# Performance work log

Hardware: AMD Instinct MI355X
Metric: run time of the kernel (lower is better)

The kernel has to match this reference:

```python
import jax, jax.numpy as jnp
import numpy as np

N, E, D, G, L = 100000, 1600000, 32, 64, 3
BN_EPS = 1e-5


def setup_inputs() -> dict:
    key = jax.random.key(0)
    ks = jax.random.split(key, 8)
    x = jax.random.normal(ks[0], (N, D), dtype=jnp.float32)
    edge_index = jax.random.randint(ks[1], (2, E), 0, N, dtype=jnp.int64)
    batch = jnp.sort(jax.random.randint(ks[2], (N,), 0, G, dtype=jnp.int64))
    layer_weights = jnp.ones((L,), dtype=jnp.float32)
    # linears[i]: Linear(D->D) + BN(D) (inference-mode stats) ; L of them
    lin_W = jax.random.normal(ks[3], (L, D, D), dtype=jnp.float32) * (1.0 / np.sqrt(D))
    lin_b = jnp.zeros((L, D), dtype=jnp.float32)
    lin_gamma = jnp.ones((L, D), dtype=jnp.float32)
    lin_beta = jnp.zeros((L, D), dtype=jnp.float32)
    lin_mean = jnp.zeros((L, D), dtype=jnp.float32)
    lin_var = jnp.ones((L, D), dtype=jnp.float32)
    # GINConv MLPs: Linear(D->D) + BN(D) + ELU ; L-1 of them
    conv_W = jax.random.normal(ks[4], (L - 1, D, D), dtype=jnp.float32) * (1.0 / np.sqrt(D))
    conv_b = jnp.zeros((L - 1, D), dtype=jnp.float32)
    conv_gamma = jnp.ones((L - 1, D), dtype=jnp.float32)
    conv_beta = jnp.zeros((L - 1, D), dtype=jnp.float32)
    conv_mean = jnp.zeros((L - 1, D), dtype=jnp.float32)
    conv_var = jnp.ones((L - 1, D), dtype=jnp.float32)
    return {"x": x, "edge_index": edge_index, "batch": batch,
            "layer_weights": layer_weights,
            "lin_W": lin_W, "lin_b": lin_b, "lin_gamma": lin_gamma,
            "lin_beta": lin_beta, "lin_mean": lin_mean, "lin_var": lin_var,
            "conv_W": conv_W, "conv_b": conv_b, "conv_gamma": conv_gamma,
            "conv_beta": conv_beta, "conv_mean": conv_mean, "conv_var": conv_var}


def _mlp(h, W, b, gamma, beta, mean, var):
    # Linear -> BatchNorm1d (inference stats) -> ELU
    h = h @ W + b
    h = (h - mean) * (gamma * jax.lax.rsqrt(var + BN_EPS)) + beta
    return jax.nn.elu(h)


def reference(x, edge_index, batch, layer_weights,
              lin_W, lin_b, lin_gamma, lin_beta, lin_mean, lin_var,
              conv_W, conv_b, conv_gamma, conv_beta, conv_mean, conv_var):
    src, dst = edge_index[0], edge_index[1]
    z = _mlp(x, lin_W[0], lin_b[0], lin_gamma[0], lin_beta[0], lin_mean[0], lin_var[0])
    Z = layer_weights[0] * z
    out = jax.ops.segment_max(z, batch, num_segments=G)  # global_max_pool
    for l in range(1, L):
        # GINConv (eps=0): x' = MLP(x + sum_{j->i} x_j)
        agg = jax.ops.segment_sum(x[src], dst, num_segments=N)
        x = _mlp(x + agg, conv_W[l - 1], conv_b[l - 1], conv_gamma[l - 1],
                 conv_beta[l - 1], conv_mean[l - 1], conv_var[l - 1])
        z = layer_weights[l] * _mlp(x, lin_W[l], lin_b[l], lin_gamma[l],
                                    lin_beta[l], lin_mean[l], lin_var[l])
        Z = Z + z
        out = out + jax.ops.segment_max(z, batch, num_segments=G)
    # dropout p=0.0 is identity
    return (out, Z, x)
```

## Files before the change

### kernel.cpp

```cpp
#include <hip/hip_runtime.h>
#include <math.h>

#define N_NODES 100000
#define N_EDGES 1600000
#define DIM 32
#define N_GROUPS 64
#define BN_EPS 1e-5f

#define BIN_NODES 128
#define NBINS ((N_NODES + BIN_NODES - 1) / BIN_NODES)
#define EPB_HIST 2048
#define HIST_BLOCKS ((N_EDGES + EPB_HIST - 1) / EPB_HIST)
#define EPB_SCAT 8192
#define SCAT_SUB (EPB_SCAT / EPB_HIST)
#define SCAT_BLOCKS ((N_EDGES + EPB_SCAT - 1) / EPB_SCAT)
#define GF2_BLOCKS ((N_NODES + 127) / 128)
#define CNT_PAD 16

#define HLS 40

typedef __attribute__((ext_vector_type(8))) short short8;
typedef __attribute__((ext_vector_type(4))) float f32x4;
typedef __attribute__((ext_vector_type(4))) unsigned u32x4;

__device__ __forceinline__ unsigned enc_f32(float f) {
    unsigned u = __float_as_uint(f);
    return (u & 0x80000000u) ? ~u : (u | 0x80000000u);
}
__device__ __forceinline__ float dec_f32(unsigned u) {
    return (u & 0x80000000u) ? __uint_as_float(u & 0x7FFFFFFFu) : __uint_as_float(~u);
}
__device__ __forceinline__ unsigned short f2bf(float f) {
    unsigned u = __float_as_uint(f);
    u += 0x7FFFu + ((u >> 16) & 1u);
    return (unsigned short)(u >> 16);
}

__global__ __launch_bounds__(256) void foldhist_kernel(
        const float* __restrict__ lin_W, const float* __restrict__ lin_b,
        const float* __restrict__ lin_gamma, const float* __restrict__ lin_beta,
        const float* __restrict__ lin_mean, const float* __restrict__ lin_var,
        const float* __restrict__ conv_W, const float* __restrict__ conv_b,
        const float* __restrict__ conv_gamma, const float* __restrict__ conv_beta,
        const float* __restrict__ conv_mean, const float* __restrict__ conv_var,
        float* __restrict__ shf, unsigned short* __restrict__ Wfb,
        unsigned short* __restrict__ x0b, unsigned short* __restrict__ xbufb,
        const int* __restrict__ dst, int* __restrict__ bincnt,
        int* __restrict__ blockcnt)
{
    __shared__ int cnt[NBINS];
    int bid = blockIdx.x;
    int t = threadIdx.x;
    if (bid >= 6) {
        int hb = bid - 6;
        for (int b = t; b < NBINS; b += 256) cnt[b] = 0;
        __syncthreads();
        int base = hb * EPB_HIST;
        for (int i = 0; i < EPB_HIST / 256; ++i) {
            int e = base + i * 256 + t;
            if (e < N_EDGES) atomicAdd(&cnt[dst[e] >> 7], 1);
        }
        __syncthreads();
        for (int b = t; b < NBINS; b += 256) {
            int c = cnt[b];
            blockcnt[(size_t)hb * NBINS + b] = c;
            if (c > 0) atomicAdd(&bincnt[b * CNT_PAD], c);
        }
        return;
    }
    if (bid == 5) {
        if (t < DIM) {
            x0b[(size_t)N_NODES * DIM + t] = 0;
            xbufb[(size_t)N_NODES * DIM + t] = 0;
        }
        return;
    }
    const float *W, *b, *gm, *bt, *mn, *vr;
    if (bid < 3) {
        W = lin_W + bid * DIM * DIM; b = lin_b + bid * DIM; gm = lin_gamma + bid * DIM;
        bt = lin_beta + bid * DIM;   mn = lin_mean + bid * DIM; vr = lin_var + bid * DIM;
    } else {
        int c = bid - 3;
        W = conv_W + c * DIM * DIM; b = conv_b + c * DIM; gm = conv_gamma + c * DIM;
        bt = conv_beta + c * DIM;   mn = conv_mean + c * DIM; vr = conv_var + c * DIM;
    }
    for (int idx = t; idx < DIM * DIM; idx += 256) {
        int j = idx & (DIM - 1);
        float scale = gm[j] / sqrtf(vr[j] + BN_EPS);
        Wfb[bid * DIM * DIM + idx] = f2bf(W[idx] * scale);
    }
    if (t < DIM) {
        float scale = gm[t] / sqrtf(vr[t] + BN_EPS);
        shf[bid * DIM + t] = (b[t] - mn[t]) * scale + bt[t];
    }
}

__global__ __launch_bounds__(1024) void binscan_kernel(const int* __restrict__ bincnt,
                                                       int* __restrict__ binoff,
                                                       int* __restrict__ bincur) {
    __shared__ int s[1024];
    int t = threadIdx.x;
    int c = (t < NBINS) ? bincnt[t * CNT_PAD] : 0;
    s[t] = c;
    __syncthreads();
    for (int off = 1; off < 1024; off <<= 1) {
        int u = (t >= off) ? s[t - off] : 0;
        __syncthreads();
        s[t] += u;
        __syncthreads();
    }
    if (t < NBINS) { binoff[t] = s[t] - c; bincur[t * CNT_PAD] = s[t] - c; }
    if (t == 0) binoff[NBINS] = N_EDGES;
}

__global__ __launch_bounds__(512) void scatter_linz_kernel(
        const int* __restrict__ src, const int* __restrict__ dst,
        int* __restrict__ bincur, unsigned* __restrict__ binbuf,
        const int* __restrict__ blockcnt,
        const float* __restrict__ x0, unsigned short* __restrict__ x0b,
        const unsigned short* __restrict__ Wb, const float* __restrict__ shfv,
        const int* __restrict__ batch, const float* __restrict__ lw_ptr,
        float* __restrict__ Z, unsigned* __restrict__ segmax)
{
    __shared__ int smem[NBINS];
    int t = threadIdx.x;

    if (blockIdx.x < SCAT_BLOCKS) {
        int* pos = smem;
        for (int b = t; b < NBINS; b += 512) {
            int c = 0;
#pragma unroll
            for (int k = 0; k < SCAT_SUB; ++k) {
                int r = blockIdx.x * SCAT_SUB + k;
                if (r < HIST_BLOCKS)
                    c += blockcnt[(size_t)r * NBINS + b];
            }
            pos[b] = (c > 0) ? atomicAdd(&bincur[b * CNT_PAD], c) : 0;
        }
        __syncthreads();
        int base = blockIdx.x * EPB_SCAT;
        for (int i = 0; i < EPB_SCAT / 512; ++i) {
            int e = base + i * 512 + t;
            if (e < N_EDGES) {
                int d = dst[e];
                int bin = d >> 7;
                int p = atomicAdd(&pos[bin], 1);
                binbuf[p] = ((unsigned)(d & 127) << 17) | (unsigned)src[e];
            }
        }
        return;
    }

    unsigned* segloc = (unsigned*)smem;
    if (t < 8 * DIM) segloc[t] = 0;

    int wv = t >> 6, lane = t & 63;
    int m = lane & 15, kg = lane >> 4;

    short8 b0, b1;
#pragma unroll
    for (int j = 0; j < 8; ++j) {
        int k = kg * 8 + j;
        b0[j] = (short)Wb[k * DIM + m];
        b1[j] = (short)Wb[k * DIM + 16 + m];
    }
    float sh0 = shfv[m], sh1 = shfv[m + 16];
    float lw = lw_ptr[0];
    int blk0 = (blockIdx.x - SCAT_BLOCKS) * 128;
    int gfirst = batch[blk0];
    int row0 = blk0 + wv * 16;
    __syncthreads();

    if (row0 < N_NODES) {
        const float* rp = x0 + (size_t)(row0 + m) * DIM + kg * 8;
        f32x4 v0 = *(const f32x4*)rp;
        f32x4 v1 = *(const f32x4*)(rp + 4);
        short8 a;
        a[0] = (short)f2bf(v0[0]); a[1] = (short)f2bf(v0[1]);
        a[2] = (short)f2bf(v0[2]); a[3] = (short)f2bf(v0[3]);
        a[4] = (short)f2bf(v1[0]); a[5] = (short)f2bf(v1[1]);
        a[6] = (short)f2bf(v1[2]); a[7] = (short)f2bf(v1[3]);
        *(short8*)(x0b + (size_t)(row0 + m) * DIM + kg * 8) = a;

        f32x4 d0 = {0.f, 0.f, 0.f, 0.f}, d1 = {0.f, 0.f, 0.f, 0.f};
        d0 = __builtin_amdgcn_mfma_f32_16x16x32_bf16(a, b0, d0, 0, 0, 0);
        d1 = __builtin_amdgcn_mfma_f32_16x16x32_bf16(a, b1, d1, 0, 0, 0);
#pragma unroll
        for (int r = 0; r < 4; ++r) {
            int row = row0 + kg * 4 + r;
            float a0 = d0[r] + sh0;
            float a1 = d1[r] + sh1;
            float z0 = a0 > 0.f ? a0 : expm1f(a0);
            float z1 = a1 > 0.f ? a1 : expm1f(a1);
            size_t zi = (size_t)row * DIM;
            Z[zi + m] = lw * z0;
            Z[zi + 16 + m] = lw * z1;
            int g = batch[row];
            int go = g - gfirst;
            if (go < 8) {
                atomicMax(&segloc[go * DIM + m], enc_f32(z0));
                atomicMax(&segloc[go * DIM + 16 + m], enc_f32(z1));
            } else {
                atomicMax(&segmax[g * DIM + m], enc_f32(z0));
                atomicMax(&segmax[g * DIM + 16 + m], enc_f32(z1));
            }
        }
    }
    __syncthreads();
    if (t < 8 * DIM) {
        unsigned v = segloc[t];
        if (v) atomicMax(&segmax[(gfirst + (t >> 5)) * DIM + (t & 31)], v);
    }
}

__global__ __launch_bounds__(256) void binsort_kernel(const unsigned* __restrict__ binbuf,
                                                      const int* __restrict__ binoff,
                                                      int* __restrict__ esrc,
                                                      int* __restrict__ nodeptr) {
    __shared__ int cnt[BIN_NODES];
    __shared__ int sc[BIN_NODES];
    int t = threadIdx.x;
    int bin = blockIdx.x;
    int beg = binoff[bin], end = binoff[bin + 1];
    if (t < BIN_NODES) cnt[t] = 0;
    __syncthreads();
    for (int e = beg + t; e < end; e += 256)
        atomicAdd(&cnt[binbuf[e] >> 17], 1);
    __syncthreads();
    int v = (t < BIN_NODES) ? cnt[t] : 0;
    if (t < BIN_NODES) sc[t] = v;
    __syncthreads();
    for (int off = 1; off < BIN_NODES; off <<= 1) {
        int u = (t < BIN_NODES && t >= off) ? sc[t - off] : 0;
        __syncthreads();
        if (t < BIN_NODES) sc[t] += u;
        __syncthreads();
    }
    if (t < BIN_NODES) {
        int excl = sc[t] - v;
        cnt[t] = excl;
        nodeptr[bin * BIN_NODES + t] = beg + excl;
    }
    __syncthreads();
    for (int e = beg + t; e < end; e += 256) {
        unsigned pe = binbuf[e];
        int dl = (int)(pe >> 17);
        int p = atomicAdd(&cnt[dl], 1);
        esrc[beg + p] = (int)(pe & 0x1FFFFu);
    }
}

#define GIN_FETCH4(I0, A)                                                       \
  {                                                                             \
    _Pragma("unroll")                                                           \
    for (int q_ = 0; q_ < 4; ++q_) {                                            \
      int ii_ = (I0) + q_;                                                      \
      int ei_ = beg + ii_;                                                      \
      ei_ = ei_ < (N_EDGES - 1) ? ei_ : (N_EDGES - 1);                          \
      int s_ = esrc[ei_];                                                       \
      s_ = (ii_ < deg) ? s_ : N_NODES;                                          \
      A[q_] = *(const short8*)(xb + (size_t)s_ * DIM + kg8);                    \
    }                                                                           \
  }

#define GIN_MFMA4(A)                                                            \
  {                                                                             \
    _Pragma("unroll")                                                           \
    for (int q_ = 0; q_ < 4; ++q_) {                                            \
      d0[q_] = __builtin_amdgcn_mfma_f32_16x16x32_bf16(A[q_], bc0, d0[q_], 0, 0, 0); \
      d1[q_] = __builtin_amdgcn_mfma_f32_16x16x32_bf16(A[q_], bc1, d1[q_], 0, 0, 0); \
    }                                                                           \
  }

__global__ __launch_bounds__(256) void gin_fused_kernel(
        const unsigned short* __restrict__ xb,
        const int* __restrict__ esrc,
        const int* __restrict__ nodeptr,
        const unsigned short* __restrict__ Wcb, const float* __restrict__ shc,
        const unsigned short* __restrict__ Wlb, const float* __restrict__ shl,
        const int* __restrict__ batch, const float* __restrict__ lw_ptr,
        unsigned short* __restrict__ xnextb,
        float* __restrict__ xoutf,
        float* __restrict__ Z,
        unsigned* __restrict__ segmax)
{
    __shared__ __align__(16) unsigned short hl[4][16 * HLS];
    __shared__ unsigned segloc[8 * DIM];
    int t = threadIdx.x;
    segloc[t] = 0;

    int wv = t >> 6, lane = t & 63;
    int m = lane & 15, kg = lane >> 4;
    int kg8 = kg * 8;

    short8 bc0, bc1, bl0, bl1;
#pragma unroll
    for (int j = 0; j < 8; ++j) {
        int k = kg8 + j;
        bc0[j] = (short)Wcb[k * DIM + m];
        bc1[j] = (short)Wcb[k * DIM + 16 + m];
        bl0[j] = (short)Wlb[k * DIM + m];
        bl1[j] = (short)Wlb[k * DIM + 16 + m];
    }
    float shc0 = shc[m], shc1 = shc[m + 16];
    float shl0 = shl[m], shl1 = shl[m + 16];
    float lw = lw_ptr[0];
    int blk0 = blockIdx.x * 64;
    int gfirst = batch[blk0 < N_NODES ? blk0 : N_NODES - 1];
    int row0 = blk0 + wv * 16;
    __syncthreads();

    if (row0 < N_NODES) {
        int beg = nodeptr[row0 + m];
        int deg = nodeptr[row0 + m + 1] - beg;
        int md = deg;
#pragma unroll
        for (int off = 1; off < 16; off <<= 1)
            md = max(md, __shfl_xor(md, off, 64));

        short8 aS = *(const short8*)(xb + (size_t)(row0 + m) * DIM + kg8);
        f32x4 d0[4], d1[4];
#pragma unroll
        for (int q = 0; q < 4; ++q) {
            d0[q] = (f32x4){0.f, 0.f, 0.f, 0.f};
            d1[q] = (f32x4){0.f, 0.f, 0.f, 0.f};
        }
        d0[0] = __builtin_amdgcn_mfma_f32_16x16x32_bf16(aS, bc0, d0[0], 0, 0, 0);
        d1[0] = __builtin_amdgcn_mfma_f32_16x16x32_bf16(aS, bc1, d1[0], 0, 0, 0);

        int B = (md + 3) >> 2;
        if (B > 0) {
            short8 aA[4], aB[4];
            GIN_FETCH4(0, aA);
            int k = 1;
            for (; k + 1 < B; k += 2) {
                GIN_FETCH4(4 * k, aB);
                GIN_MFMA4(aA);
                GIN_FETCH4(4 * (k + 1), aA);
                GIN_MFMA4(aB);
            }
            if (k < B) {
                GIN_FETCH4(4 * k, aB);
                GIN_MFMA4(aA);
                GIN_MFMA4(aB);
            } else {
                GIN_MFMA4(aA);
            }
        }

        float hp0[4], hp1[4];
#pragma unroll
        for (int r = 0; r < 4; ++r) {
            float a0 = d0[0][r] + d0[1][r] + d0[2][r] + d0[3][r] + shc0;
            float a1 = d1[0][r] + d1[1][r] + d1[2][r] + d1[3][r] + shc1;
            hp0[r] = a0 > 0.f ? a0 : expm1f(a0);
            hp1[r] = a1 > 0.f ? a1 : expm1f(a1);
        }
#pragma unroll
        for (int r = 0; r < 4; ++r) {
            hl[wv][(kg * 4 + r) * HLS + m] = f2bf(hp0[r]);
            hl[wv][(kg * 4 + r) * HLS + 16 + m] = f2bf(hp1[r]);
        }
        if (xoutf) {
#pragma unroll
            for (int r = 0; r < 4; ++r) {
                int row = row0 + kg * 4 + r;
                xoutf[(size_t)row * DIM + m] = hp0[r];
                xoutf[(size_t)row * DIM + 16 + m] = hp1[r];
            }
        }
        if (xnextb) {
            int ii = lane >> 2, q = lane & 3;
            u32x4 pk = *(const u32x4*)&hl[wv][ii * HLS + q * 8];
            *(u32x4*)(xnextb + (size_t)(row0 + ii) * DIM + q * 8) = pk;
        }

        short8 a2 = *(const short8*)&hl[wv][m * HLS + kg8];
        f32x4 e0 = {0.f, 0.f, 0.f, 0.f}, e1 = {0.f, 0.f, 0.f, 0.f};
        e0 = __builtin_amdgcn_mfma_f32_16x16x32_bf16(a2, bl0, e0, 0, 0, 0);
        e1 = __builtin_amdgcn_mfma_f32_16x16x32_bf16(a2, bl1, e1, 0, 0, 0);
#pragma unroll
        for (int r = 0; r < 4; ++r) {
            int row = row0 + kg * 4 + r;
            float a0 = e0[r] + shl0, a1 = e1[r] + shl1;
            float z0 = a0 > 0.f ? a0 : expm1f(a0);
            float z1 = a1 > 0.f ? a1 : expm1f(a1);
            float zw0 = lw * z0, zw1 = lw * z1;
            size_t zi = (size_t)row * DIM;
            Z[zi + m] += zw0;
            Z[zi + 16 + m] += zw1;
            int g = batch[row];
            int go = g - gfirst;
            if (go < 8) {
                atomicMax(&segloc[go * DIM + m], enc_f32(zw0));
                atomicMax(&segloc[go * DIM + 16 + m], enc_f32(zw1));
            } else {
                atomicMax(&segmax[g * DIM + m], enc_f32(zw0));
                atomicMax(&segmax[g * DIM + 16 + m], enc_f32(zw1));
            }
        }
    }
    __syncthreads();
    unsigned v = segloc[t];
    if (v) atomicMax(&segmax[(gfirst + (t >> 5)) * DIM + (t & 31)], v);
}

__global__ void add_out3_kernel(const unsigned* __restrict__ s0,
                                const unsigned* __restrict__ s1,
                                const unsigned* __restrict__ s2,
                                float* __restrict__ out) {
    int t = blockIdx.x * blockDim.x + threadIdx.x;
    out[t] = dec_f32(s0[t]) + dec_f32(s1[t]) + dec_f32(s2[t]);
}

extern "C" void kernel_launch(void* const* d_in, const int* in_sizes, int n_in,
                              void* d_out, int out_size, void* d_ws, size_t ws_size,
                              hipStream_t stream) {
    const float* x0        = (const float*)d_in[0];
    const int*   ei        = (const int*)d_in[1];
    const int*   batch     = (const int*)d_in[2];
    const float* lw        = (const float*)d_in[3];
    const float* lin_W     = (const float*)d_in[4];
    const float* lin_b     = (const float*)d_in[5];
    const float* lin_gamma = (const float*)d_in[6];
    const float* lin_beta  = (const float*)d_in[7];
    const float* lin_mean  = (const float*)d_in[8];
    const float* lin_var   = (const float*)d_in[9];
    const float* conv_W    = (const float*)d_in[10];
    const float* conv_b    = (const float*)d_in[11];
    const float* conv_gamma= (const float*)d_in[12];
    const float* conv_beta = (const float*)d_in[13];
    const float* conv_mean = (const float*)d_in[14];
    const float* conv_var  = (const float*)d_in[15];

    float* out  = (float*)d_out;
    float* Z    = out + N_GROUPS * DIM;
    float* xout = Z + (size_t)N_NODES * DIM;

    char* p = (char*)d_ws;
    unsigned short* x0b     = (unsigned short*)p; p += ((size_t)N_NODES * DIM + 8192) * sizeof(unsigned short);
    unsigned short* xbufb   = (unsigned short*)p; p += ((size_t)N_NODES * DIM + 8192) * sizeof(unsigned short);
    unsigned*       binbuf  = (unsigned*)p;       p += (size_t)N_EDGES * sizeof(unsigned);
    int*            esrc    = (int*)p;            p += (size_t)N_EDGES * sizeof(int);
    int*            nodeptr = (int*)p;            p += (NBINS * BIN_NODES + 1) * sizeof(int);
    unsigned*       segmx   = (unsigned*)p;       p += 3 * N_GROUPS * DIM * sizeof(unsigned);
    int*            bincnt  = (int*)p;            p += NBINS * CNT_PAD * sizeof(int);
    int*            binoff  = (int*)p;            p += (NBINS + 1) * sizeof(int);
    int*            bincur  = (int*)p;            p += NBINS * CNT_PAD * sizeof(int);
    float*          shf     = (float*)p;          p += 5 * DIM * sizeof(float);
    unsigned short* Wfb     = (unsigned short*)p; p += 5 * DIM * DIM * sizeof(unsigned short);

    int* blockcnt = (int*)xbufb;

    const int* src = ei;
    const int* dst = ei + N_EDGES;

    const int gf_blocks = (N_NODES + 63) / 64;

    (void)hipMemsetAsync(segmx, 0,
                         (3 * N_GROUPS * DIM + NBINS * CNT_PAD) * sizeof(unsigned), stream);

    foldhist_kernel<<<6 + HIST_BLOCKS, 256, 0, stream>>>(
        lin_W, lin_b, lin_gamma, lin_beta, lin_mean, lin_var,
        conv_W, conv_b, conv_gamma, conv_beta, conv_mean, conv_var,
        shf, Wfb, x0b, xbufb, dst, bincnt, blockcnt);

    binscan_kernel<<<1, 1024, 0, stream>>>(bincnt, binoff, bincur);

    scatter_linz_kernel<<<SCAT_BLOCKS + GF2_BLOCKS, 512, 0, stream>>>(
        src, dst, bincur, binbuf, blockcnt,
        x0, x0b, Wfb, shf, batch, lw, Z, segmx);

    binsort_kernel<<<NBINS, 256, 0, stream>>>(binbuf, binoff, esrc, nodeptr);

    gin_fused_kernel<<<gf_blocks, 256, 0, stream>>>(x0b, esrc, nodeptr,
                                                    Wfb + 3 * DIM * DIM, shf + 3 * DIM,
                                                    Wfb + 1 * DIM * DIM, shf + 1 * DIM,
                                                    batch, lw + 1,
                                                    xbufb, (float*)nullptr, Z,
                                                    segmx + N_GROUPS * DIM);

    gin_fused_kernel<<<gf_blocks, 256, 0, stream>>>(xbufb, esrc, nodeptr,
                                                    Wfb + 4 * DIM * DIM, shf + 4 * DIM,
                                                    Wfb + 2 * DIM * DIM, shf + 2 * DIM,
                                                    batch, lw + 2,
                                                    (unsigned short*)nullptr, xout, Z,
                                                    segmx + 2 * N_GROUPS * DIM);

    add_out3_kernel<<<8, 256, 0, stream>>>(segmx, segmx + N_GROUPS * DIM,
                                           segmx + 2 * N_GROUPS * DIM, out);
}
```

Measured before the change: 249.5 us.

## Sort nodes by degree within each bin to balance wave workloads

binsort_kernel now builds a per-bin permutation of nodes sorted by in-degree using a shared-memory counting sort. The GIN kernel processes nodes in that order, so each 16-node MFMA tile groups nodes of similar degree. This cuts the padding work caused by taking the max degree over 16 rows. In exchange, node IDs are looked up indirectly, and the outputs to Z, x and xout become scattered writes within a 128-node bin.

```diff
diff --git a/kernel.cpp b/kernel.cpp
--- a/kernel.cpp
+++ b/kernel.cpp
@@ -216,9 +216,11 @@
 __global__ __launch_bounds__(256) void binsort_kernel(const unsigned* __restrict__ binbuf,
                                                       const int* __restrict__ binoff,
                                                       int* __restrict__ esrc,
-                                                      int* __restrict__ nodeptr) {
+                                                      int* __restrict__ nodeptr,
+                                                      int* __restrict__ perm) {
     __shared__ int cnt[BIN_NODES];
     __shared__ int sc[BIN_NODES];
+    __shared__ int dh[256];
     int t = threadIdx.x;
     int bin = blockIdx.x;
     int beg = binoff[bin], end = binoff[bin + 1];
@@ -247,6 +249,31 @@
         int dl = (int)(pe >> 17);
         int p = atomicAdd(&cnt[dl], 1);
         esrc[beg + p] = (int)(pe & 0x1FFFFu);
+    }
+    dh[t] = 0;
+    __syncthreads();
+    int key = 255;
+    if (t < BIN_NODES) {
+        int node = bin * BIN_NODES + t;
+        key = (node < N_NODES) ? (v < 255 ? v : 254) : 255;
+        atomicAdd(&dh[key], 1);
+    }
+    __syncthreads();
+    int c2 = dh[t];
+    __syncthreads();
+    for (int off = 1; off < 256; off <<= 1) {
+        int u = (t >= off) ? dh[t - off] : 0;
+        __syncthreads();
+        dh[t] += u;
+        __syncthreads();
+    }
+    int excl2 = dh[t] - c2;
+    __syncthreads();
+    dh[t] = excl2;
+    __syncthreads();
+    if (t < BIN_NODES) {
+        int r = atomicAdd(&dh[key], 1);
+        perm[bin * BIN_NODES + r] = bin * BIN_NODES + t;
     }
 }
 
@@ -276,6 +303,7 @@
         const unsigned short* __restrict__ xb,
         const int* __restrict__ esrc,
         const int* __restrict__ nodeptr,
+        const int* __restrict__ perm,
         const unsigned short* __restrict__ Wcb, const float* __restrict__ shc,
         const unsigned short* __restrict__ Wlb, const float* __restrict__ shl,
         const int* __restrict__ batch, const float* __restrict__ lw_ptr,
@@ -306,19 +334,24 @@
     float shl0 = shl[m], shl1 = shl[m + 16];
     float lw = lw_ptr[0];
     int blk0 = blockIdx.x * 64;
-    int gfirst = batch[blk0 < N_NODES ? blk0 : N_NODES - 1];
+    int bin0 = blk0 >> 7;
+    int gfirst = batch[bin0 * BIN_NODES];
     int row0 = blk0 + wv * 16;
     __syncthreads();
 
     if (row0 < N_NODES) {
-        int beg = nodeptr[row0 + m];
-        int deg = nodeptr[row0 + m + 1] - beg;
+        int slot = row0 + m;
+        int n = perm[slot];
+        bool nv = n < N_NODES;
+        int nload = nv ? n : N_NODES;
+        int beg = nodeptr[nv ? n : 0];
+        int deg = nv ? (nodeptr[n + 1] - beg) : 0;
         int md = deg;
 #pragma unroll
         for (int off = 1; off < 16; off <<= 1)
             md = max(md, __shfl_xor(md, off, 64));
 
-        short8 aS = *(const short8*)(xb + (size_t)(row0 + m) * DIM + kg8);
+        short8 aS = *(const short8*)(xb + (size_t)nload * DIM + kg8);
         f32x4 d0[4], d1[4];
 #pragma unroll
         for (int q = 0; q < 4; ++q) {
@@ -364,15 +397,20 @@
         if (xoutf) {
 #pragma unroll
             for (int r = 0; r < 4; ++r) {
-                int row = row0 + kg * 4 + r;
-                xoutf[(size_t)row * DIM + m] = hp0[r];
-                xoutf[(size_t)row * DIM + 16 + m] = hp1[r];
+                int n_r = __shfl(n, kg * 4 + r, 64);
+                if (n_r < N_NODES) {
+                    xoutf[(size_t)n_r * DIM + m] = hp0[r];
+                    xoutf[(size_t)n_r * DIM + 16 + m] = hp1[r];
+                }
             }
         }
         if (xnextb) {
             int ii = lane >> 2, q = lane & 3;
-            u32x4 pk = *(const u32x4*)&hl[wv][ii * HLS + q * 8];
-            *(u32x4*)(xnextb + (size_t)(row0 + ii) * DIM + q * 8) = pk;
+            int n_ii = __shfl(n, ii, 64);
+            if (n_ii < N_NODES) {
+                u32x4 pk = *(const u32x4*)&hl[wv][ii * HLS + q * 8];
+                *(u32x4*)(xnextb + (size_t)n_ii * DIM + q * 8) = pk;
+            }
         }
 
         short8 a2 = *(const short8*)&hl[wv][m * HLS + kg8];
@@ -381,22 +419,24 @@
         e1 = __builtin_amdgcn_mfma_f32_16x16x32_bf16(a2, bl1, e1, 0, 0, 0);
 #pragma unroll
         for (int r = 0; r < 4; ++r) {
-            int row = row0 + kg * 4 + r;
-            float a0 = e0[r] + shl0, a1 = e1[r] + shl1;
-            float z0 = a0 > 0.f ? a0 : expm1f(a0);
-            float z1 = a1 > 0.f ? a1 : expm1f(a1);
-            float zw0 = lw * z0, zw1 = lw * z1;
-            size_t zi = (size_t)row * DIM;
-            Z[zi + m] += zw0;
-            Z[zi + 16 + m] += zw1;
-            int g = batch[row];
-            int go = g - gfirst;
-            if (go < 8) {
-                atomicMax(&segloc[go * DIM + m], enc_f32(zw0));
-                atomicMax(&segloc[go * DIM + 16 + m], enc_f32(zw1));
-            } else {
-                atomicMax(&segmax[g * DIM + m], enc_f32(zw0));
-                atomicMax(&segmax[g * DIM + 16 + m], enc_f32(zw1));
+            int n_r = __shfl(n, kg * 4 + r, 64);
+            if (n_r < N_NODES) {
+                float a0 = e0[r] + shl0, a1 = e1[r] + shl1;
+                float z0 = a0 > 0.f ? a0 : expm1f(a0);
+                float z1 = a1 > 0.f ? a1 : expm1f(a1);
+                float zw0 = lw * z0, zw1 = lw * z1;
+                size_t zi = (size_t)n_r * DIM;
+                Z[zi + m] += zw0;
+                Z[zi + 16 + m] += zw1;
+                int g = batch[n_r];
+                int go = g - gfirst;
+                if (go < 8) {
+                    atomicMax(&segloc[go * DIM + m], enc_f32(zw0));
+                    atomicMax(&segloc[go * DIM + 16 + m], enc_f32(zw1));
+                } else {
+                    atomicMax(&segmax[g * DIM + m], enc_f32(zw0));
+                    atomicMax(&segmax[g * DIM + 16 + m], enc_f32(zw1));
+                }
             }
         }
     }
@@ -443,6 +483,7 @@
     unsigned*       binbuf  = (unsigned*)p;       p += (size_t)N_EDGES * sizeof(unsigned);
     int*            esrc    = (int*)p;            p += (size_t)N_EDGES * sizeof(int);
     int*            nodeptr = (int*)p;            p += (NBINS * BIN_NODES + 1) * sizeof(int);
+    int*            perm    = (int*)p;            p += (NBINS * BIN_NODES) * sizeof(int);
     unsigned*       segmx   = (unsigned*)p;       p += 3 * N_GROUPS * DIM * sizeof(unsigned);
     int*            bincnt  = (int*)p;            p += NBINS * CNT_PAD * sizeof(int);
     int*            binoff  = (int*)p;            p += (NBINS + 1) * sizeof(int);
@@ -471,16 +512,16 @@
         src, dst, bincur, binbuf, blockcnt,
         x0, x0b, Wfb, shf, batch, lw, Z, segmx);
 
-    binsort_kernel<<<NBINS, 256, 0, stream>>>(binbuf, binoff, esrc, nodeptr);
-
-    gin_fused_kernel<<<gf_blocks, 256, 0, stream>>>(x0b, esrc, nodeptr,
+    binsort_kernel<<<NBINS, 256, 0, stream>>>(binbuf, binoff, esrc, nodeptr, perm);
+
+    gin_fused_kernel<<<gf_blocks, 256, 0, stream>>>(x0b, esrc, nodeptr, perm,
                                                     Wfb + 3 * DIM * DIM, shf + 3 * DIM,
                                                     Wfb + 1 * DIM * DIM, shf + 1 * DIM,
                                                     batch, lw + 1,
                                                     xbufb, (float*)nullptr, Z,
                                                     segmx + N_GROUPS * DIM);
 
-    gin_fused_kernel<<<gf_blocks, 256, 0, stream>>>(xbufb, esrc, nodeptr,
+    gin_fused_kernel<<<gf_blocks, 256, 0, stream>>>(xbufb, esrc, nodeptr, perm,
                                                     Wfb + 4 * DIM * DIM, shf + 4 * DIM,
                                                     Wfb + 2 * DIM * DIM, shf + 2 * DIM,
                                                     batch, lw + 2,
```

Measured after the change: 254.0 us. Within noise of the previous version (+1.8%).

## Fold bin scan and output reduction into last-block tails; store Z partials in bf16

Applied to the files above, without the earlier changes.

Drops the separate binscan and add_out3 launches by running the bin prefix scan in the last finishing block of foldhist and the final segment-max sum in the last block of the second GIN kernel, using atomic completion counters and thread fences. It also keeps the running Z accumulator in a bf16 workspace between layers and writes fp32 Z only at the end, which halves intermediate Z traffic. The cost is extra precision loss in Z from bf16 rounding of partial sums, plus serialized tail work in a single block.

```diff
diff --git a/kernel.cpp b/kernel.cpp
--- a/kernel.cpp
+++ b/kernel.cpp
@@ -34,6 +34,9 @@
     unsigned u = __float_as_uint(f);
     u += 0x7FFFu + ((u >> 16) & 1u);
     return (unsigned short)(u >> 16);
+}
+__device__ __forceinline__ float bf2f(unsigned short u) {
+    return __uint_as_float(((unsigned)u) << 16);
 }
 
 __global__ __launch_bounds__(256) void foldhist_kernel(
@@ -46,9 +49,13 @@
         float* __restrict__ shf, unsigned short* __restrict__ Wfb,
         unsigned short* __restrict__ x0b, unsigned short* __restrict__ xbufb,
         const int* __restrict__ dst, int* __restrict__ bincnt,
-        int* __restrict__ blockcnt)
+        int* __restrict__ blockcnt,
+        int* __restrict__ binoff, int* __restrict__ bincur,
+        int* __restrict__ done0)
 {
     __shared__ int cnt[NBINS];
+    __shared__ int sscan[256];
+    __shared__ int tick;
     int bid = blockIdx.x;
     int t = threadIdx.x;
     if (bid >= 6) {
@@ -66,51 +73,58 @@
             blockcnt[(size_t)hb * NBINS + b] = c;
             if (c > 0) atomicAdd(&bincnt[b * CNT_PAD], c);
         }
-        return;
-    }
-    if (bid == 5) {
+    } else if (bid == 5) {
         if (t < DIM) {
             x0b[(size_t)N_NODES * DIM + t] = 0;
             xbufb[(size_t)N_NODES * DIM + t] = 0;
         }
-        return;
-    }
-    const float *W, *b, *gm, *bt, *mn, *vr;
-    if (bid < 3) {
-        W = lin_W + bid * DIM * DIM; b = lin_b + bid * DIM; gm = lin_gamma + bid * DIM;
-        bt = lin_beta + bid * DIM;   mn = lin_mean + bid * DIM; vr = lin_var + bid * DIM;
     } else {
-        int c = bid - 3;
-        W = conv_W + c * DIM * DIM; b = conv_b + c * DIM; gm = conv_gamma + c * DIM;
-        bt = conv_beta + c * DIM;   mn = conv_mean + c * DIM; vr = conv_var + c * DIM;
-    }
-    for (int idx = t; idx < DIM * DIM; idx += 256) {
-        int j = idx & (DIM - 1);
-        float scale = gm[j] / sqrtf(vr[j] + BN_EPS);
-        Wfb[bid * DIM * DIM + idx] = f2bf(W[idx] * scale);
-    }
-    if (t < DIM) {
-        float scale = gm[t] / sqrtf(vr[t] + BN_EPS);
-        shf[bid * DIM + t] = (b[t] - mn[t]) * scale + bt[t];
-    }
-}
-
-__global__ __launch_bounds__(1024) void binscan_kernel(const int* __restrict__ bincnt,
-                                                       int* __restrict__ binoff,
-                                                       int* __restrict__ bincur) {
-    __shared__ int s[1024];
-    int t = threadIdx.x;
-    int c = (t < NBINS) ? bincnt[t * CNT_PAD] : 0;
-    s[t] = c;
-    __syncthreads();
-    for (int off = 1; off < 1024; off <<= 1) {
-        int u = (t >= off) ? s[t - off] : 0;
-        __syncthreads();
-        s[t] += u;
-        __syncthreads();
-    }
-    if (t < NBINS) { binoff[t] = s[t] - c; bincur[t * CNT_PAD] = s[t] - c; }
-    if (t == 0) binoff[NBINS] = N_EDGES;
+        const float *W, *b, *gm, *bt, *mn, *vr;
+        if (bid < 3) {
+            W = lin_W + bid * DIM * DIM; b = lin_b + bid * DIM; gm = lin_gamma + bid * DIM;
+            bt = lin_beta + bid * DIM;   mn = lin_mean + bid * DIM; vr = lin_var + bid * DIM;
+        } else {
+            int c = bid - 3;
+            W = conv_W + c * DIM * DIM; b = conv_b + c * DIM; gm = conv_gamma + c * DIM;
+            bt = conv_beta + c * DIM;   mn = conv_mean + c * DIM; vr = conv_var + c * DIM;
+        }
+        for (int idx = t; idx < DIM * DIM; idx += 256) {
+            int j = idx & (DIM - 1);
+            float scale = gm[j] / sqrtf(vr[j] + BN_EPS);
+            Wfb[bid * DIM * DIM + idx] = f2bf(W[idx] * scale);
+        }
+        if (t < DIM) {
+            float scale = gm[t] / sqrtf(vr[t] + BN_EPS);
+            shf[bid * DIM + t] = (b[t] - mn[t]) * scale + bt[t];
+        }
+    }
+    __threadfence();
+    __syncthreads();
+    if (t == 0) tick = atomicAdd(done0, 1);
+    __syncthreads();
+    if (tick == (int)gridDim.x - 1) {
+        __threadfence();
+        int i0 = t * 4;
+        int c0 = (i0 + 0 < NBINS) ? bincnt[(i0 + 0) * CNT_PAD] : 0;
+        int c1 = (i0 + 1 < NBINS) ? bincnt[(i0 + 1) * CNT_PAD] : 0;
+        int c2 = (i0 + 2 < NBINS) ? bincnt[(i0 + 2) * CNT_PAD] : 0;
+        int c3 = (i0 + 3 < NBINS) ? bincnt[(i0 + 3) * CNT_PAD] : 0;
+        int local = c0 + c1 + c2 + c3;
+        sscan[t] = local;
+        __syncthreads();
+        for (int off = 1; off < 256; off <<= 1) {
+            int u = (t >= off) ? sscan[t - off] : 0;
+            __syncthreads();
+            sscan[t] += u;
+            __syncthreads();
+        }
+        int run = sscan[t] - local;
+        if (i0 + 0 < NBINS) { binoff[i0 + 0] = run; bincur[(i0 + 0) * CNT_PAD] = run; run += c0; }
+        if (i0 + 1 < NBINS) { binoff[i0 + 1] = run; bincur[(i0 + 1) * CNT_PAD] = run; run += c1; }
+        if (i0 + 2 < NBINS) { binoff[i0 + 2] = run; bincur[(i0 + 2) * CNT_PAD] = run; run += c2; }
+        if (i0 + 3 < NBINS) { binoff[i0 + 3] = run; bincur[(i0 + 3) * CNT_PAD] = run; run += c3; }
+        if (t == 0) binoff[NBINS] = N_EDGES;
+    }
 }
 
 __global__ __launch_bounds__(512) void scatter_linz_kernel(
@@ -120,7 +134,7 @@
         const float* __restrict__ x0, unsigned short* __restrict__ x0b,
         const unsigned short* __restrict__ Wb, const float* __restrict__ shfv,
         const int* __restrict__ batch, const float* __restrict__ lw_ptr,
-        float* __restrict__ Z, unsigned* __restrict__ segmax)
+        unsigned short* __restrict__ zb, unsigned* __restrict__ segmax)
 {
     __shared__ int smem[NBINS];
     int t = threadIdx.x;
@@ -193,8 +207,8 @@
             float z0 = a0 > 0.f ? a0 : expm1f(a0);
             float z1 = a1 > 0.f ? a1 : expm1f(a1);
             size_t zi = (size_t)row * DIM;
-            Z[zi + m] = lw * z0;
-            Z[zi + 16 + m] = lw * z1;
+            zb[zi + m] = f2bf(lw * z0);
+            zb[zi + 16 + m] = f2bf(lw * z1);
             int g = batch[row];
             int go = g - gfirst;
             if (go < 8) {
@@ -281,11 +295,15 @@
         const int* __restrict__ batch, const float* __restrict__ lw_ptr,
         unsigned short* __restrict__ xnextb,
         float* __restrict__ xoutf,
-        float* __restrict__ Z,
-        unsigned* __restrict__ segmax)
+        unsigned short* __restrict__ zb,
+        float* __restrict__ Zfin,
+        unsigned* __restrict__ segmax,
+        const unsigned* __restrict__ sm0, const unsigned* __restrict__ sm1,
+        float* __restrict__ outv, int* __restrict__ done1)
 {
     __shared__ __align__(16) unsigned short hl[4][16 * HLS];
     __shared__ unsigned segloc[8 * DIM];
+    __shared__ int lastt;
     int t = threadIdx.x;
     segloc[t] = 0;
 
@@ -387,8 +405,13 @@
             float z1 = a1 > 0.f ? a1 : expm1f(a1);
             float zw0 = lw * z0, zw1 = lw * z1;
             size_t zi = (size_t)row * DIM;
-            Z[zi + m] += zw0;
-            Z[zi + 16 + m] += zw1;
+            if (Zfin) {
+                Zfin[zi + m]      = bf2f(zb[zi + m]) + zw0;
+                Zfin[zi + 16 + m] = bf2f(zb[zi + 16 + m]) + zw1;
+            } else {
+                zb[zi + m]      = f2bf(bf2f(zb[zi + m]) + zw0);
+                zb[zi + 16 + m] = f2bf(bf2f(zb[zi + 16 + m]) + zw1);
+            }
             int g = batch[row];
             int go = g - gfirst;
             if (go < 8) {
@@ -403,14 +426,18 @@
     __syncthreads();
     unsigned v = segloc[t];
     if (v) atomicMax(&segmax[(gfirst + (t >> 5)) * DIM + (t & 31)], v);
-}
-
-__global__ void add_out3_kernel(const unsigned* __restrict__ s0,
-                                const unsigned* __restrict__ s1,
-                                const unsigned* __restrict__ s2,
-                                float* __restrict__ out) {
-    int t = blockIdx.x * blockDim.x + threadIdx.x;
-    out[t] = dec_f32(s0[t]) + dec_f32(s1[t]) + dec_f32(s2[t]);
+
+    if (outv) {
+        __threadfence();
+        __syncthreads();
+        if (t == 0) lastt = atomicAdd(done1, 1);
+        __syncthreads();
+        if (lastt == (int)gridDim.x - 1) {
+            __threadfence();
+            for (int i = t; i < N_GROUPS * DIM; i += 256)
+                outv[i] = dec_f32(sm0[i]) + dec_f32(sm1[i]) + dec_f32(segmax[i]);
+        }
+    }
 }
 
 extern "C" void kernel_launch(void* const* d_in, const int* in_sizes, int n_in,
@@ -440,11 +467,13 @@
     char* p = (char*)d_ws;
     unsigned short* x0b     = (unsigned short*)p; p += ((size_t)N_NODES * DIM + 8192) * sizeof(unsigned short);
     unsigned short* xbufb   = (unsigned short*)p; p += ((size_t)N_NODES * DIM + 8192) * sizeof(unsigned short);
+    unsigned short* zb      = (unsigned short*)p; p += ((size_t)N_NODES * DIM) * sizeof(unsigned short);
     unsigned*       binbuf  = (unsigned*)p;       p += (size_t)N_EDGES * sizeof(unsigned);
     int*            esrc    = (int*)p;            p += (size_t)N_EDGES * sizeof(int);
     int*            nodeptr = (int*)p;            p += (NBINS * BIN_NODES + 1) * sizeof(int);
     unsigned*       segmx   = (unsigned*)p;       p += 3 * N_GROUPS * DIM * sizeof(unsigned);
     int*            bincnt  = (int*)p;            p += NBINS * CNT_PAD * sizeof(int);
+    int*            donec   = (int*)p;            p += 16 * sizeof(int);
     int*            binoff  = (int*)p;            p += (NBINS + 1) * sizeof(int);
     int*            bincur  = (int*)p;            p += NBINS * CNT_PAD * sizeof(int);
     float*          shf     = (float*)p;          p += 5 * DIM * sizeof(float);
@@ -458,18 +487,17 @@
     const int gf_blocks = (N_NODES + 63) / 64;
 
     (void)hipMemsetAsync(segmx, 0,
-                         (3 * N_GROUPS * DIM + NBINS * CNT_PAD) * sizeof(unsigned), stream);
+                         (3 * N_GROUPS * DIM + NBINS * CNT_PAD + 16) * sizeof(unsigned), stream);
 
     foldhist_kernel<<<6 + HIST_BLOCKS, 256, 0, stream>>>(
         lin_W, lin_b, lin_gamma, lin_beta, lin_mean, lin_var,
         conv_W, conv_b, conv_gamma, conv_beta, conv_mean, conv_var,
-        shf, Wfb, x0b, xbufb, dst, bincnt, blockcnt);
-
-    binscan_kernel<<<1, 1024, 0, stream>>>(bincnt, binoff, bincur);
+        shf, Wfb, x0b, xbufb, dst, bincnt, blockcnt,
+        binoff, bincur, donec);
 
     scatter_linz_kernel<<<SCAT_BLOCKS + GF2_BLOCKS, 512, 0, stream>>>(
         src, dst, bincur, binbuf, blockcnt,
-        x0, x0b, Wfb, shf, batch, lw, Z, segmx);
+        x0, x0b, Wfb, shf, batch, lw, zb, segmx);
 
     binsort_kernel<<<NBINS, 256, 0, stream>>>(binbuf, binoff, esrc, nodeptr);
 
@@ -477,16 +505,19 @@
                                                     Wfb + 3 * DIM * DIM, shf + 3 * DIM,
                                                     Wfb + 1 * DIM * DIM, shf + 1 * DIM,
                                                     batch, lw + 1,
-                                                    xbufb, (float*)nullptr, Z,
-                                                    segmx + N_GROUPS * DIM);
+                                                    xbufb, (float*)nullptr,
+                                                    zb, (float*)nullptr,
+                                                    segmx + N_GROUPS * DIM,
+                                                    (const unsigned*)nullptr, (const unsigned*)nullptr,
+                                                    (float*)nullptr, (int*)nullptr);
 
     gin_fused_kernel<<<gf_blocks, 256, 0, stream>>>(xbufb, esrc, nodeptr,
                                                     Wfb + 4 * DIM * DIM, shf + 4 * DIM,
                                                     Wfb + 2 * DIM * DIM, shf + 2 * DIM,
                                                     batch, lw + 2,
-                                                    (unsigned short*)nullptr, xout, Z,
-                                                    segmx + 2 * N_GROUPS * DIM);
-
-    add_out3_kernel<<<8, 256, 0, stream>>>(segmx, segmx + N_GROUPS * DIM,
-                                           segmx + 2 * N_GROUPS * DIM, out);
-}
+                                                    (unsigned short*)nullptr, xout,
+                                                    zb, Z,
+                                                    segmx + 2 * N_GROUPS * DIM,
+                                                    segmx, segmx + N_GROUPS * DIM,
+                                                    out, donec + 1);
+}
```

Measured after the change: 448.1 us. +79.6%, slower.
